# Kernel tuning notes

Measured on AMD Instinct MI355X. Metric: run time of the kernel, lower is better.

The kernel has to match this reference:

```python
import jax, jax.numpy as jnp
import numpy as np

HEADS = 16

def _rotate_half(t):
    t1, t2 = jnp.split(t, 2, axis=-1)
    return jnp.concatenate([-t2, t1], axis=-1)

def _apply_rope(q, k, sin, cos):
    # sin/cos: [Lp, hd] -> broadcast to [1,1,Lp,hd]
    sin = sin[None, None, :, :]
    cos = cos[None, None, :, :]
    q = q * cos + _rotate_half(q) * sin
    k = k * cos + _rotate_half(k) * sin
    return q, k

def setup_inputs() -> dict:
    key = jax.random.key(0)
    ks = jax.random.split(key, 6)
    B, L, C = 16, 1025, 1024
    hd = C // HEADS
    x = jax.random.normal(ks[0], (B, L, C), dtype=jnp.float32)
    sin = jax.random.uniform(ks[1], (L - 1, hd), dtype=jnp.float32)
    cos = jax.random.uniform(ks[2], (L - 1, hd), dtype=jnp.float32)
    qkv_w = jax.random.normal(ks[3], (3 * C, C), dtype=jnp.float32) * 0.02
    proj_w = jax.random.normal(ks[4], (C, C), dtype=jnp.float32) * 0.02
    proj_b = jnp.zeros((C,), dtype=jnp.float32)
    return {"x": x, "sin": sin, "cos": cos, "qkv_w": qkv_w, "proj_w": proj_w, "proj_b": proj_b}

def reference(x, sin, cos, qkv_w, proj_w, proj_b):
    B, L, C = x.shape
    H = HEADS
    hd = C // H
    scale = hd ** (-0.5)
    # QKV projection (no bias), split into heads: [3, B, H, L, hd]
    qkv = (x @ qkv_w.T).reshape(B, L, 3, H, hd).transpose(2, 0, 3, 1, 4)
    q, k, v = qkv[0], qkv[1], qkv[2]
    # L == sin.shape[0] + 1 -> CLS token split, RoPE on patch tokens only
    q_cls, q_patch = q[:, :, :1], q[:, :, 1:]
    k_cls, k_patch = k[:, :, :1], k[:, :, 1:]
    q_patch, k_patch = _apply_rope(q_patch, k_patch, sin, cos)
    q = jnp.concatenate([q_cls, q_patch], axis=2)
    k = jnp.concatenate([k_cls, k_patch], axis=2)
    attn = jnp.einsum("bhqd,bhkd->bhqk", q, k) * scale
    attn = jax.nn.softmax(attn, axis=-1)
    out = jnp.einsum("bhqk,bhkd->bhqd", attn, v)  # [B,H,L,hd]
    out = out.transpose(0, 2, 1, 3).reshape(B, L, C)
    return out @ proj_w.T + proj_b
```

## Files before the change

### kernel.cpp

```cpp
#include <hip/hip_runtime.h>

typedef unsigned short ushort_t;
typedef unsigned int uint_t;
typedef __attribute__((ext_vector_type(8))) short short8;
typedef __attribute__((ext_vector_type(4))) float f32x4;

#define Bv 16
#define Lv 1025
#define LpD 1088
#define Cv 1024
#define Hv 16
#define BHv 256
#define Mv 16400
#define Mp 16512

#define MFMA(a, b, c) __builtin_amdgcn_mfma_f32_16x16x32_bf16(a, b, c, 0, 0, 0)

__device__ __forceinline__ ushort_t f2b(float x) {
    uint_t r;
    asm("v_cvt_pk_bf16_f32 %0, %1, %1" : "=v"(r) : "v"(x));
    return (ushort_t)r;
}
__device__ __forceinline__ float b2f(ushort_t v) {
    return __uint_as_float(((uint_t)v) << 16);
}
__device__ __forceinline__ uint_t pk2(float a, float b) {
    uint_t r;
    asm("v_cvt_pk_bf16_f32 %0, %1, %2" : "=v"(r) : "v"(a), "v"(b));
    return r;
}
__device__ __forceinline__ float fexp2(float x) {
    float r;
    asm("v_exp_f32 %0, %1" : "=v"(r) : "v"(x));
    return r;
}

__device__ __forceinline__ void gl2lds16(const ushort_t* g, void* lds) {
    __builtin_amdgcn_global_load_lds(
        (const __attribute__((address_space(1))) void*)g,
        (__attribute__((address_space(3))) void*)lds, 16, 0, 0);
}

__device__ __forceinline__ short8 frag(const ushort_t* base, int row, int chunk) {
    return *(const short8*)(base + row * 64 + ((chunk ^ (row & 7)) << 3));
}

__global__ __launch_bounds__(256) void conv_bf16(const float* __restrict__ s,
                                                 ushort_t* __restrict__ d,
                                                 int n_valid, int n_total) {
    int i = (blockIdx.x * 256 + threadIdx.x) * 4;
    if (i >= n_total) return;
    float4 v = make_float4(0.f, 0.f, 0.f, 0.f);
    if (i < n_valid) v = *(const float4*)(s + i);
    uint2 o;
    o.x = pk2(v.x, v.y);
    o.y = pk2(v.z, v.w);
    *(uint2*)(d + i) = o;
}

__global__ __launch_bounds__(256, 4) void gemm_qkv(const ushort_t* __restrict__ A,
                                                   const ushort_t* __restrict__ W,
                                                   ushort_t* __restrict__ Q,
                                                   ushort_t* __restrict__ K,
                                                   ushort_t* __restrict__ V,
                                                   const float* __restrict__ sinp,
                                                   const float* __restrict__ cosp) {
    __shared__ uint4 sm[2112];
    ushort_t* As = (ushort_t*)sm;
    ushort_t* Bs = As + 128 * 64;
    const int t = threadIdx.x;
    const int w = t >> 6, l = t & 63;
    const int m0 = blockIdx.y * 128, n0 = blockIdx.x * 128;
    const int wm = (w >> 1) * 64, wn = (w & 1) * 64;
    const int srow = (w * 32) + (l >> 3);
    const int scs = (l & 7) ^ (srow & 7);
    f32x4 acc[4][4] = {};
    for (int k0 = 0; k0 < 1024; k0 += 64) {
        __syncthreads();
#pragma unroll
        for (int i = 0; i < 4; i++) {
            int row = srow + i * 8;
            gl2lds16(A + (size_t)(m0 + row) * 1024 + k0 + scs * 8,
                     As + (w * 32 + i * 8) * 64);
            gl2lds16(W + (size_t)(n0 + row) * 1024 + k0 + scs * 8,
                     Bs + (w * 32 + i * 8) * 64);
        }
        __syncthreads();
#pragma unroll
        for (int kb = 0; kb < 2; kb++) {
            short8 af[4], bf[4];
#pragma unroll
            for (int mb = 0; mb < 4; mb++)
                af[mb] = frag(As, wm + mb * 16 + (l & 15), kb * 4 + (l >> 4));
#pragma unroll
            for (int nb = 0; nb < 4; nb++)
                bf[nb] = frag(Bs, wn + nb * 16 + (l & 15), kb * 4 + (l >> 4));
#pragma unroll
            for (int mb = 0; mb < 4; mb++)
#pragma unroll
                for (int nb = 0; nb < 4; nb++)
                    acc[mb][nb] = MFMA(af[mb], bf[nb], acc[mb][nb]);
        }
    }
    __syncthreads();
    ushort_t (*St)[132] = (ushort_t(*)[132])sm;
#pragma unroll
    for (int mb = 0; mb < 4; mb++)
#pragma unroll
        for (int r = 0; r < 4; r++)
#pragma unroll
            for (int nb = 0; nb < 4; nb++)
                St[wm + mb * 16 + (l >> 4) * 4 + r][wn + nb * 16 + (l & 15)] =
                    f2b(acc[mb][nb][r]);
    __syncthreads();
#pragma unroll
    for (int it = 0; it < 8; it++) {
        int seg = it * 32 + w * 8 + (l >> 3);
        int mr = seg >> 1, p = seg & 1;
        int m = m0 + mr;
        if (m >= Mv) continue;
        int b = m / 1025, lseq = m - b * 1025;
        int n = n0 + p * 64;
        int which = n >> 10, h = (n >> 6) & 15;
        ushort_t* dst = (which == 0) ? Q : ((which == 1) ? K : V);
        const int d0 = (l & 7) * 8;
        size_t doff = ((size_t)(b * Hv + h) * LpD + lseq) * 64 + d0;
        if (which <= 1 && lseq > 0) {
            const ushort_t* rowp = &St[mr][p * 64];
            const float* cw = cosp + (lseq - 1) * 64 + d0;
            const float* sw = sinp + (lseq - 1) * 64 + d0;
            float4 c0 = *(const float4*)cw, c1 = *(const float4*)(cw + 4);
            float4 s0 = *(const float4*)sw, s1 = *(const float4*)(sw + 4);
            float cc[8] = {c0.x, c0.y, c0.z, c0.w, c1.x, c1.y, c1.z, c1.w};
            float ss[8] = {s0.x, s0.y, s0.z, s0.w, s1.x, s1.y, s1.z, s1.w};
            float sgn = (d0 < 32) ? -1.f : 1.f;
            uint_t ov[4];
#pragma unroll
            for (int jj = 0; jj < 4; jj++) {
                float f0 = b2f(rowp[d0 + jj * 2]);
                float f1 = b2f(rowp[d0 + jj * 2 + 1]);
                float r0 = b2f(rowp[(d0 ^ 32) + jj * 2]) * sgn;
                float r1 = b2f(rowp[(d0 ^ 32) + jj * 2 + 1]) * sgn;
                ov[jj] = pk2(f0 * cc[jj * 2] + r0 * ss[jj * 2],
                             f1 * cc[jj * 2 + 1] + r1 * ss[jj * 2 + 1]);
            }
            *(uint4*)(dst + doff) = *(uint4*)ov;
        } else {
            *(uint4*)(dst + doff) = *(const uint4*)&St[mr][p * 64 + d0];
        }
    }
}

__global__ __launch_bounds__(256) void transpose_v(const ushort_t* __restrict__ Vb,
                                                   ushort_t* __restrict__ Vt) {
    __shared__ ushort_t Ts[64][72];
    const int t = threadIdx.x;
    const int l0 = blockIdx.x * 64, bh = blockIdx.y;
#pragma unroll
    for (int i = 0; i < 2; i++) {
        int c = t + 256 * i; int row = c >> 3, cir = c & 7;
        uint4 v = make_uint4(0u, 0u, 0u, 0u);
        if (l0 + row < Lv)
            v = *(const uint4*)(Vb + ((size_t)bh * LpD + l0 + row) * 64 + cir * 8);
        *(uint4*)&Ts[row][cir * 8] = v;
    }
    __syncthreads();
#pragma unroll
    for (int i = 0; i < 2; i++) {
        int c = t + 256 * i; int d = c >> 3, lg = c & 7;
        short8 v;
#pragma unroll
        for (int j = 0; j < 8; j++) v[j] = (short)Ts[lg * 8 + j][d];
        *(short8*)(Vt + ((size_t)bh * 64 + d) * LpD + l0 + lg * 8) = v;
    }
}

__global__ __launch_bounds__(256, 4) void attn_mfma(const ushort_t* __restrict__ Qb,
                                                    const ushort_t* __restrict__ Kb,
                                                    const ushort_t* __restrict__ Vt,
                                                    ushort_t* __restrict__ AO) {
    __shared__ ushort_t QP[64 * 64];
    __shared__ ushort_t Kd[2][64 * 64];
    __shared__ ushort_t Vd[2][64 * 64];
    const int t = threadIdx.x, w = t >> 6, l = t & 63;
    const int wg = blockIdx.x;
    const int nid = (wg & 7) * 544 + (wg >> 3);
    const int bh = nid / 17, qt = nid - bh * 17;
    const int q0 = qt * 64;
    const size_t kbase = (size_t)bh * LpD * 64;
    const size_t vbase = (size_t)bh * 64 * LpD;
    const int scs = (l & 7) ^ ((l >> 3) & 7);
    const int g = l >> 4;
    const int qr = l & 15;
    const int q7 = l & 7;

#pragma unroll
    for (int i = 0; i < 2; i++) {
        int row = w * 16 + i * 8 + (l >> 3);
        gl2lds16(Qb + kbase + (size_t)(q0 + row) * 64 + scs * 8,
                 QP + (w * 16 + i * 8) * 64);
    }
#pragma unroll
    for (int i = 0; i < 2; i++) {
        int row = w * 16 + i * 8 + (l >> 3);
        gl2lds16(Kb + kbase + (size_t)row * 64 + scs * 8,
                 Kd[0] + (w * 16 + i * 8) * 64);
        gl2lds16(Vt + vbase + (size_t)row * LpD + scs * 8,
                 Vd[0] + (w * 16 + i * 8) * 64);
    }
    asm volatile("s_waitcnt vmcnt(4)" ::: "memory");
    asm volatile("s_barrier" ::: "memory");
    short8 aq0 = frag(QP, w * 16 + qr, g);
    short8 aq1 = frag(QP, w * 16 + qr, 4 + g);
    asm volatile("s_waitcnt lgkmcnt(0)" ::: "memory");

    ushort_t* prow = QP + (w * 16 + qr) * 64;

    short8 ones;
#pragma unroll
    for (int j = 0; j < 8; j++) ones[j] = (short)0x3F80;
    f32x4 o[4] = {};
    f32x4 sacc = {};
    const float CE = 0.18033688011112042f;

    for (int kt = 0; kt < 17; kt++) {
        const ushort_t* Ks = Kd[kt & 1];
        const ushort_t* Vs = Vd[kt & 1];
        if (kt < 16) {
#pragma unroll
            for (int i = 0; i < 2; i++) {
                int row = w * 16 + i * 8 + (l >> 3);
                gl2lds16(Kb + kbase + (size_t)((kt + 1) * 64 + row) * 64 + scs * 8,
                         Kd[(kt + 1) & 1] + (w * 16 + i * 8) * 64);
                gl2lds16(Vt + vbase + (size_t)row * LpD + (kt + 1) * 64 + scs * 8,
                         Vd[(kt + 1) & 1] + (w * 16 + i * 8) * 64);
            }
            asm volatile("s_waitcnt vmcnt(4)" ::: "memory");
        } else {
            asm volatile("s_waitcnt vmcnt(0)" ::: "memory");
        }
        asm volatile("s_barrier" ::: "memory");
#pragma unroll
        for (int cb = 0; cb < 4; cb++) {
            short8 bk0 = frag(Ks, cb * 16 + qr, g);
            short8 bk1 = frag(Ks, cb * 16 + qr, 4 + g);
            f32x4 s = {};
            s = MFMA(bk0, aq0, s);
            s = MFMA(bk1, aq1, s);
            float p4[4];
#pragma unroll
            for (int r = 0; r < 4; r++) p4[r] = fexp2(s[r] * CE);
            if (kt == 16) {
                bool keep0 = (cb == 0) && (g == 0);
                p4[0] = keep0 ? p4[0] : 0.f;
                p4[1] = 0.f; p4[2] = 0.f; p4[3] = 0.f;
            }
            uint2 pw;
            pw.x = pk2(p4[0], p4[1]);
            pw.y = pk2(p4[2], p4[3]);
            *(uint2*)(prow + (((2 * cb + (g >> 1)) ^ q7) << 3) + ((g & 1) << 2)) = pw;
        }
        short8 ap0 = *(const short8*)(prow + ((g ^ q7) << 3));
        short8 ap1 = *(const short8*)(prow + (((4 + g) ^ q7) << 3));
        __builtin_amdgcn_s_setprio(1);
        sacc = MFMA(ap0, ones, sacc);
        sacc = MFMA(ap1, ones, sacc);
#pragma unroll
        for (int cb = 0; cb < 4; cb++) {
            short8 bv0 = frag(Vs, cb * 16 + qr, g);
            short8 bv1 = frag(Vs, cb * 16 + qr, 4 + g);
            o[cb] = MFMA(ap0, bv0, o[cb]);
            o[cb] = MFMA(ap1, bv1, o[cb]);
        }
        __builtin_amdgcn_s_setprio(0);
        asm volatile("s_barrier" ::: "memory");
    }
    const int b = bh >> 4, h = bh & 15;
#pragma unroll
    for (int r = 0; r < 4; r++) {
        int lq = q0 + w * 16 + g * 4 + r;
        if (lq >= Lv) continue;
        float inv = 1.f / sacc[r];
        size_t ob = ((size_t)(b * 1025 + lq)) * 1024 + h * 64;
#pragma unroll
        for (int cb = 0; cb < 4; cb++)
            AO[ob + cb * 16 + qr] = f2b(o[cb][r] * inv);
    }
}

__global__ __launch_bounds__(256, 4) void gemm_proj(const ushort_t* __restrict__ A,
                                                    const ushort_t* __restrict__ W,
                                                    const float* __restrict__ bias,
                                                    float* __restrict__ out) {
    __shared__ uint4 sm[2112];
    ushort_t* As = (ushort_t*)sm;
    ushort_t* Bs = As + 128 * 64;
    const int t = threadIdx.x;
    const int w = t >> 6, l = t & 63;
    const int m0 = blockIdx.y * 128, n0 = blockIdx.x * 128;
    const int wm = (w >> 1) * 64, wn = (w & 1) * 64;
    const int srow = (w * 32) + (l >> 3);
    const int scs = (l & 7) ^ (srow & 7);
    f32x4 acc[4][4] = {};
    for (int k0 = 0; k0 < 1024; k0 += 64) {
        __syncthreads();
#pragma unroll
        for (int i = 0; i < 4; i++) {
            int row = srow + i * 8;
            gl2lds16(A + (size_t)(m0 + row) * 1024 + k0 + scs * 8,
                     As + (w * 32 + i * 8) * 64);
            gl2lds16(W + (size_t)(n0 + row) * 1024 + k0 + scs * 8,
                     Bs + (w * 32 + i * 8) * 64);
        }
        __syncthreads();
#pragma unroll
        for (int kb = 0; kb < 2; kb++) {
            short8 af[4], bf[4];
#pragma unroll
            for (int mb = 0; mb < 4; mb++)
                af[mb] = frag(As, wm + mb * 16 + (l & 15), kb * 4 + (l >> 4));
#pragma unroll
            for (int nb = 0; nb < 4; nb++)
                bf[nb] = frag(Bs, wn + nb * 16 + (l & 15), kb * 4 + (l >> 4));
#pragma unroll
            for (int mb = 0; mb < 4; mb++)
#pragma unroll
                for (int nb = 0; nb < 4; nb++)
                    acc[mb][nb] = MFMA(af[mb], bf[nb], acc[mb][nb]);
        }
    }
    float bias4[4];
#pragma unroll
    for (int nb = 0; nb < 4; nb++) bias4[nb] = bias[n0 + wn + nb * 16 + (l & 15)];
    float (*Sf)[132] = (float(*)[132])sm;
#pragma unroll
    for (int half = 0; half < 2; half++) {
        __syncthreads();
        if ((w >> 1) == half) {
#pragma unroll
            for (int mb = 0; mb < 4; mb++)
#pragma unroll
                for (int r = 0; r < 4; r++)
#pragma unroll
                    for (int nb = 0; nb < 4; nb++)
                        Sf[mb * 16 + (l >> 4) * 4 + r][wn + nb * 16 + (l & 15)] =
                            acc[mb][nb][r] + bias4[nb];
        }
        __syncthreads();
#pragma unroll
        for (int it = 0; it < 8; it++) {
            int rr = it * 8 + w * 2 + (l >> 5);
            int m = m0 + half * 64 + rr;
            if (m < Mv)
                *(float4*)(out + (size_t)m * 1024 + n0 + (l & 31) * 4) =
                    *(const float4*)&Sf[rr][(l & 31) * 4];
        }
    }
}

extern "C" void kernel_launch(void* const* d_in, const int* in_sizes, int n_in,
                              void* d_out, int out_size, void* d_ws, size_t ws_size,
                              hipStream_t stream) {
    (void)in_sizes; (void)n_in; (void)out_size; (void)ws_size;
    const float* x      = (const float*)d_in[0];
    const float* sinp   = (const float*)d_in[1];
    const float* cosp   = (const float*)d_in[2];
    const float* qkv_w  = (const float*)d_in[3];
    const float* proj_w = (const float*)d_in[4];
    const float* proj_b = (const float*)d_in[5];
    float* out = (float*)d_out;

    const size_t SZH = (size_t)BHv * LpD * 64;
    ushort_t* xb  = (ushort_t*)d_ws;
    ushort_t* qwb = xb + (size_t)Mp * 1024;
    ushort_t* pwb = qwb + (size_t)3072 * 1024;
    ushort_t* Qb  = pwb + (size_t)1024 * 1024;
    ushort_t* Kb  = Qb + SZH;
    ushort_t* Vb  = Kb + SZH;
    ushort_t* Vt  = Vb + SZH;
    ushort_t* AO  = Vt + SZH;

    dim3 blk(256);
    conv_bf16<<<dim3(Mp * 1024 / 1024), blk, 0, stream>>>(x, xb, Mv * 1024, Mp * 1024);
    conv_bf16<<<dim3(3072 * 1024 / 1024), blk, 0, stream>>>(qkv_w, qwb, 3072 * 1024, 3072 * 1024);
    conv_bf16<<<dim3(1024 * 1024 / 1024), blk, 0, stream>>>(proj_w, pwb, 1024 * 1024, 1024 * 1024);
    gemm_qkv<<<dim3(24, 129), blk, 0, stream>>>(xb, qwb, Qb, Kb, Vb, sinp, cosp);
    transpose_v<<<dim3(17, BHv), blk, 0, stream>>>(Vb, Vt);
    attn_mfma<<<dim3(17 * BHv), blk, 0, stream>>>(Qb, Kb, Vt, AO);
    gemm_proj<<<dim3(8, 129), blk, 0, stream>>>(AO, pwb, proj_b, out);
}
```

Baseline: 438.8 us.

## Double attention query tile to 128 rows with 512-thread blocks sharing K/V tiles

The attention kernel now processes 128 query rows per block with 8 waves instead of 64 rows with 4 waves, so each K/V tile loaded into LDS serves twice as many queries and global K/V traffic is halved. Q gets its own padded layout (LpQ=1152) plus a new kernel that zeroes the padding rows, and each wave now issues one K and one V async copy per tile. The attention output buffer reuses the bf16 x workspace to save memory. Larger blocks raise LDS and register pressure per block and may lower occupancy, and the last query tile carries more padding work.

```diff
diff --git a/kernel.cpp b/kernel.cpp
--- a/kernel.cpp
+++ b/kernel.cpp
@@ -8,6 +8,7 @@
 #define Bv 16
 #define Lv 1025
 #define LpD 1088
+#define LpQ 1152
 #define Cv 1024
 #define Hv 16
 #define BHv 256
@@ -56,6 +57,14 @@
     o.x = pk2(v.x, v.y);
     o.y = pk2(v.z, v.w);
     *(uint2*)(d + i) = o;
+}
+
+__global__ __launch_bounds__(256) void zero_qpad(ushort_t* __restrict__ Qb) {
+    int e8 = (blockIdx.x * 256 + threadIdx.x) * 8;
+    int bh = e8 / 8128;
+    int rem = e8 - bh * 8128;
+    *(uint4*)(Qb + (size_t)bh * LpQ * 64 + (size_t)Lv * 64 + rem) =
+        make_uint4(0u, 0u, 0u, 0u);
 }
 
 __global__ __launch_bounds__(256, 4) void gemm_qkv(const ushort_t* __restrict__ A,
@@ -123,8 +132,9 @@
         int n = n0 + p * 64;
         int which = n >> 10, h = (n >> 6) & 15;
         ushort_t* dst = (which == 0) ? Q : ((which == 1) ? K : V);
+        const size_t stride = (which == 0) ? (size_t)LpQ : (size_t)LpD;
         const int d0 = (l & 7) * 8;
-        size_t doff = ((size_t)(b * Hv + h) * LpD + lseq) * 64 + d0;
+        size_t doff = ((size_t)(b * Hv + h) * stride + lseq) * 64 + d0;
         if (which <= 1 && lseq > 0) {
             const ushort_t* rowp = &St[mr][p * 64];
             const float* cw = cosp + (lseq - 1) * 64 + d0;
@@ -175,18 +185,19 @@
     }
 }
 
-__global__ __launch_bounds__(256, 4) void attn_mfma(const ushort_t* __restrict__ Qb,
+__global__ __launch_bounds__(512, 6) void attn_mfma(const ushort_t* __restrict__ Qb,
                                                     const ushort_t* __restrict__ Kb,
                                                     const ushort_t* __restrict__ Vt,
                                                     ushort_t* __restrict__ AO) {
-    __shared__ ushort_t QP[64 * 64];
+    __shared__ ushort_t QP[128 * 64];
     __shared__ ushort_t Kd[2][64 * 64];
     __shared__ ushort_t Vd[2][64 * 64];
     const int t = threadIdx.x, w = t >> 6, l = t & 63;
     const int wg = blockIdx.x;
-    const int nid = (wg & 7) * 544 + (wg >> 3);
-    const int bh = nid / 17, qt = nid - bh * 17;
-    const int q0 = qt * 64;
+    const int nid = (wg & 7) * 288 + (wg >> 3);
+    const int bh = nid / 9, qt = nid - bh * 9;
+    const int q0 = qt * 128;
+    const size_t qbase = (size_t)bh * LpQ * 64;
     const size_t kbase = (size_t)bh * LpD * 64;
     const size_t vbase = (size_t)bh * 64 * LpD;
     const int scs = (l & 7) ^ ((l >> 3) & 7);
@@ -197,18 +208,15 @@
 #pragma unroll
     for (int i = 0; i < 2; i++) {
         int row = w * 16 + i * 8 + (l >> 3);
-        gl2lds16(Qb + kbase + (size_t)(q0 + row) * 64 + scs * 8,
+        gl2lds16(Qb + qbase + (size_t)(q0 + row) * 64 + scs * 8,
                  QP + (w * 16 + i * 8) * 64);
     }
-#pragma unroll
-    for (int i = 0; i < 2; i++) {
-        int row = w * 16 + i * 8 + (l >> 3);
-        gl2lds16(Kb + kbase + (size_t)row * 64 + scs * 8,
-                 Kd[0] + (w * 16 + i * 8) * 64);
-        gl2lds16(Vt + vbase + (size_t)row * LpD + scs * 8,
-                 Vd[0] + (w * 16 + i * 8) * 64);
-    }
-    asm volatile("s_waitcnt vmcnt(4)" ::: "memory");
+    {
+        int row = w * 8 + (l >> 3);
+        gl2lds16(Kb + kbase + (size_t)row * 64 + scs * 8, Kd[0] + (w * 8) * 64);
+        gl2lds16(Vt + vbase + (size_t)row * LpD + scs * 8, Vd[0] + (w * 8) * 64);
+    }
+    asm volatile("s_waitcnt vmcnt(2)" ::: "memory");
     asm volatile("s_barrier" ::: "memory");
     short8 aq0 = frag(QP, w * 16 + qr, g);
     short8 aq1 = frag(QP, w * 16 + qr, 4 + g);
@@ -227,15 +235,12 @@
         const ushort_t* Ks = Kd[kt & 1];
         const ushort_t* Vs = Vd[kt & 1];
         if (kt < 16) {
-#pragma unroll
-            for (int i = 0; i < 2; i++) {
-                int row = w * 16 + i * 8 + (l >> 3);
-                gl2lds16(Kb + kbase + (size_t)((kt + 1) * 64 + row) * 64 + scs * 8,
-                         Kd[(kt + 1) & 1] + (w * 16 + i * 8) * 64);
-                gl2lds16(Vt + vbase + (size_t)row * LpD + (kt + 1) * 64 + scs * 8,
-                         Vd[(kt + 1) & 1] + (w * 16 + i * 8) * 64);
-            }
-            asm volatile("s_waitcnt vmcnt(4)" ::: "memory");
+            int row = w * 8 + (l >> 3);
+            gl2lds16(Kb + kbase + (size_t)((kt + 1) * 64 + row) * 64 + scs * 8,
+                     Kd[(kt + 1) & 1] + (w * 8) * 64);
+            gl2lds16(Vt + vbase + (size_t)row * LpD + (kt + 1) * 64 + scs * 8,
+                     Vd[(kt + 1) & 1] + (w * 8) * 64);
+            asm volatile("s_waitcnt vmcnt(2)" ::: "memory");
         } else {
             asm volatile("s_waitcnt vmcnt(0)" ::: "memory");
         }
@@ -370,22 +375,24 @@
     const float* proj_b = (const float*)d_in[5];
     float* out = (float*)d_out;
 
+    const size_t SZQ = (size_t)BHv * LpQ * 64;
     const size_t SZH = (size_t)BHv * LpD * 64;
     ushort_t* xb  = (ushort_t*)d_ws;
     ushort_t* qwb = xb + (size_t)Mp * 1024;
     ushort_t* pwb = qwb + (size_t)3072 * 1024;
     ushort_t* Qb  = pwb + (size_t)1024 * 1024;
-    ushort_t* Kb  = Qb + SZH;
+    ushort_t* Kb  = Qb + SZQ;
     ushort_t* Vb  = Kb + SZH;
     ushort_t* Vt  = Vb + SZH;
-    ushort_t* AO  = Vt + SZH;
+    ushort_t* AO  = xb;
 
     dim3 blk(256);
     conv_bf16<<<dim3(Mp * 1024 / 1024), blk, 0, stream>>>(x, xb, Mv * 1024, Mp * 1024);
     conv_bf16<<<dim3(3072 * 1024 / 1024), blk, 0, stream>>>(qkv_w, qwb, 3072 * 1024, 3072 * 1024);
     conv_bf16<<<dim3(1024 * 1024 / 1024), blk, 0, stream>>>(proj_w, pwb, 1024 * 1024, 1024 * 1024);
+    zero_qpad<<<dim3(1016), blk, 0, stream>>>(Qb);
     gemm_qkv<<<dim3(24, 129), blk, 0, stream>>>(xb, qwb, Qb, Kb, Vb, sinp, cosp);
     transpose_v<<<dim3(17, BHv), blk, 0, stream>>>(Vb, Vt);
-    attn_mfma<<<dim3(17 * BHv), blk, 0, stream>>>(Qb, Kb, Vt, AO);
+    attn_mfma<<<dim3(9 * BHv), dim3(512), 0, stream>>>(Qb, Kb, Vt, AO);
     gemm_proj<<<dim3(8, 129), blk, 0, stream>>>(AO, pwb, proj_b, out);
 }
```

New measurement: 433.2 us. Within noise of the previous version (-1.3%).
